# Kernel tuning notes

Hardware: AMD Instinct MI355X
Metric: run time of the kernel (lower is better)

The kernel has to match this reference:

```python
import jax, jax.numpy as jnp
import numpy as np

HIDDEN = 2048
HEADS = 16
HEAD_DIM = HIDDEN // HEADS
THETA = 10000.0


def _rope(x, seq_len):
    # x: [B, S, H, Dh]; standard rotate-half RoPE (cos1==cos2, sin1==sin2 in source)
    d = x.shape[-1]
    inv_freq = 1.0 / (THETA ** (jnp.arange(0, d, 2, dtype=jnp.float32) / d))  # [Dh/2]
    freqs = jnp.arange(seq_len, dtype=jnp.float32)[:, None] * inv_freq[None, :]  # [S, Dh/2]
    cos = jnp.cos(freqs)[None, :, None, :]  # [1,S,1,Dh/2]
    sin = jnp.sin(freqs)[None, :, None, :]
    x1, x2 = x[..., : d // 2], x[..., d // 2 :]
    return jnp.concatenate([x1 * cos - x2 * sin, x1 * sin + x2 * cos], axis=-1)


def setup_inputs() -> dict:
    key = jax.random.key(0)
    ks = jax.random.split(key, 5)
    B, S = 2, 2048
    scale = 1.0 / np.sqrt(HIDDEN)
    return {
        "x": jax.random.normal(ks[0], (B, S, HIDDEN), dtype=jnp.float32),
        "Wq": jax.random.normal(ks[1], (HIDDEN, HIDDEN), dtype=jnp.float32) * scale,
        "Wk": jax.random.normal(ks[2], (HIDDEN, HIDDEN), dtype=jnp.float32) * scale,
        "Wv": jax.random.normal(ks[3], (HIDDEN, HIDDEN), dtype=jnp.float32) * scale,
        "Wo": jax.random.normal(ks[4], (HIDDEN, HIDDEN), dtype=jnp.float32) * scale,
    }


def reference(x, Wq, Wk, Wv, Wo):
    B, S, _ = x.shape
    # nn.Linear(bias=False): y = x @ W.T
    q = (x @ Wq.T).reshape(B, S, HEADS, HEAD_DIM)
    k = (x @ Wk.T).reshape(B, S, HEADS, HEAD_DIM)
    v = (x @ Wv.T).reshape(B, S, HEADS, HEAD_DIM)
    q = _rope(q, S)
    k = _rope(k, S)
    # [B,H,S,S] scores
    scores = jnp.einsum("bqhd,bkhd->bhqk", q, k) / jnp.sqrt(jnp.float32(HEAD_DIM))
    attn = jax.nn.softmax(scores, axis=-1)
    out = jnp.einsum("bhqk,bkhd->bqhd", attn, v).reshape(B, S, HIDDEN)
    return out @ Wo.T
```

## Files before the change

kernel.cpp:

```cpp
#include <hip/hip_runtime.h>
#include <hip/hip_bf16.h>


typedef __attribute__((ext_vector_type(8))) short short8;
typedef __attribute__((ext_vector_type(4))) float f32x4;
typedef __attribute__((ext_vector_type(4))) unsigned short us4;
typedef __attribute__((ext_vector_type(4))) unsigned int u32x4;

__device__ __forceinline__ void gll16(const void* g, void* l) {
  __builtin_amdgcn_global_load_lds((const __attribute__((address_space(1))) void*)g,
                                   (__attribute__((address_space(3))) void*)l, 16, 0, 0);
}

__device__ __forceinline__ unsigned short f2bf(float f) {
  __hip_bfloat16 h = __float2bfloat16(f);
  return *reinterpret_cast<unsigned short*>(&h);
}

__device__ __forceinline__ float bf2f(short s) {
  union { unsigned int u; float f; } c;
  c.u = ((unsigned int)(unsigned short)s) << 16;
  return c.f;
}

__device__ __forceinline__ unsigned int cvtpk(float lo, float hi) {
  unsigned int r;
  asm("v_cvt_pk_bf16_f32 %0, %1, %2" : "=v"(r) : "v"(lo), "v"(hi));
  return r;
}

__device__ __forceinline__ void xcd_remap(int& Bx, int& By) {
  const int flat = blockIdx.y * gridDim.x + blockIdx.x;
  const int xcd = flat & 7, idx = flat >> 3;
  const int ppx = gridDim.y >> 3;
  By = xcd * ppx + (idx % ppx);
  Bx = idx / ppx;
}

__global__ __launch_bounds__(256) void cast5(const float* __restrict__ x,
                                             const float* __restrict__ wq,
                                             const float* __restrict__ wk,
                                             const float* __restrict__ wv,
                                             const float* __restrict__ wo,
                                             __hip_bfloat16* __restrict__ xb,
                                             __hip_bfloat16* __restrict__ dq,
                                             __hip_bfloat16* __restrict__ dk,
                                             __hip_bfloat16* __restrict__ dv,
                                             __hip_bfloat16* __restrict__ dwo,
                                             int nx4, int nw4) {
  int i = blockIdx.x * 256 + threadIdx.x;
  const float* in;
  __hip_bfloat16* out;
  int j = i;
  if (i < nx4) { in = x; out = xb; }
  else if ((j = i - nx4) < nw4) { in = wq; out = dq; }
  else if ((j -= nw4) < nw4) { in = wk; out = dk; }
  else if ((j -= nw4) < nw4) { in = wv; out = dv; }
  else if ((j -= nw4) < nw4) { in = wo; out = dwo; }
  else return;
  const float4 v = reinterpret_cast<const float4*>(in)[j];
  us4 o;
  o[0] = f2bf(v.x); o[1] = f2bf(v.y); o[2] = f2bf(v.z); o[3] = f2bf(v.w);
  *reinterpret_cast<us4*>(out + (size_t)j * 4) = o;
}

template <typename EPI>
__device__ __forceinline__ void gemm_core(const __hip_bfloat16* A, const __hip_bfloat16* Bt,
                                          int row0, int col0, int K, EPI epi) {
  __shared__ char As[2][16384];
  __shared__ char Bs[2][16384];
  const int tid = threadIdx.x;
  const int lane = tid & 63, wid = tid >> 6;
  const int l15 = lane & 15, l4 = lane >> 4;
  const int wm = (wid >> 1) * 64, wn = (wid & 1) * 64;

  f32x4 acc[4][4] = {};

  const int rs = lane >> 3;
  const int cs = lane & 7;
  const int cg = cs ^ rs;
  const char* Ab = (const char*)A;
  const char* Bb = (const char*)Bt;
  const size_t Kb = (size_t)K * 2;
  const int NT = K >> 6;

#define GSTAGE(T, S)                                                                      \
  {                                                                                       \
    const int k0_ = (T) << 6;                                                             \
    _Pragma("unroll") for (int c_ = 0; c_ < 4; ++c_) {                                    \
      const int cid_ = wid * 4 + c_;                                                      \
      const int r_ = cid_ * 8 + rs;                                                       \
      gll16(Ab + (size_t)(row0 + r_) * Kb + (size_t)k0_ * 2 + cg * 16, As[S] + cid_ * 1024); \
      gll16(Bb + (size_t)(col0 + r_) * Kb + (size_t)k0_ * 2 + cg * 16, Bs[S] + cid_ * 1024); \
    }                                                                                     \
  }

  GSTAGE(0, 0);
  GSTAGE(1, 1);
  asm volatile("s_waitcnt vmcnt(8)" ::: "memory");
  __builtin_amdgcn_s_barrier();

  for (int t = 0; t < NT; ++t) {
    const int s = t & 1;
    short8 a[2][4], b[2][4];
#pragma unroll
    for (int kc = 0; kc < 2; ++kc)
#pragma unroll
      for (int i = 0; i < 4; ++i) {
        const int ra = wm + i * 16 + l15;
        a[kc][i] = *(const short8*)(As[s] + ra * 128 + (((kc * 4 + l4) ^ (ra & 7)) * 16));
        const int rb = wn + i * 16 + l15;
        b[kc][i] = *(const short8*)(Bs[s] + rb * 128 + (((kc * 4 + l4) ^ (rb & 7)) * 16));
      }
    asm volatile("s_waitcnt lgkmcnt(0)" ::: "memory");
    __builtin_amdgcn_sched_barrier(0);
    __builtin_amdgcn_s_barrier();
    if (t + 2 < NT) {
      GSTAGE(t + 2, s);
      asm volatile("s_waitcnt vmcnt(8)" ::: "memory");
    } else if (t + 2 == NT) {
      asm volatile("s_waitcnt vmcnt(0)" ::: "memory");
    }
    __builtin_amdgcn_s_barrier();
#pragma unroll
    for (int kc = 0; kc < 2; ++kc) {
      __builtin_amdgcn_s_setprio(1);
#pragma unroll
      for (int i = 0; i < 4; ++i)
#pragma unroll
        for (int j = 0; j < 4; ++j)
          acc[i][j] = __builtin_amdgcn_mfma_f32_16x16x32_bf16(a[kc][i], b[kc][j], acc[i][j], 0, 0, 0);
      __builtin_amdgcn_s_setprio(0);
    }
  }
  epi(acc, wm, wn, l15, l4);
#undef GSTAGE
}

template <int MODE>
__global__ __launch_bounds__(256) void gemm_bt(const __hip_bfloat16* __restrict__ A,
                                               const __hip_bfloat16* __restrict__ Bt,
                                               void* __restrict__ Cout,
                                               int M, int N, int K) {
  int Bx, By;
  xcd_remap(Bx, By);
  const int row0 = Bx * 128, col0 = By * 128;
  gemm_core(A, Bt, row0, col0, K, [=](f32x4 (&acc)[4][4], int wm, int wn, int l15, int l4) {
    if (MODE == 2) {
      __hip_bfloat16* vt = (__hip_bfloat16*)Cout;
#pragma unroll
      for (int i = 0; i < 4; ++i) {
        const int gm = row0 + wm + i * 16 + l4 * 4;
        const int bb = gm >> 11, kvb = gm & 2047;
        const int phys = (kvb & ~31) + (((kvb >> 2) & 3) << 3) + (((kvb >> 4) & 1) << 2);
#pragma unroll
        for (int j = 0; j < 4; ++j) {
          const int gn = col0 + wn + j * 16 + l15;
          const int h = gn >> 7, d = gn & 127;
          us4 o;
          o[0] = f2bf(acc[i][j][0]); o[1] = f2bf(acc[i][j][1]);
          o[2] = f2bf(acc[i][j][2]); o[3] = f2bf(acc[i][j][3]);
          *reinterpret_cast<us4*>(vt + ((size_t)((bb * 16 + h) * 128 + d) * 2048 + phys)) = o;
        }
      }
    } else {
#pragma unroll
      for (int i = 0; i < 4; ++i)
#pragma unroll
        for (int j = 0; j < 4; ++j) {
          const int gn = col0 + wn + j * 16 + l15;
#pragma unroll
          for (int r = 0; r < 4; ++r) {
            const int gm = row0 + wm + i * 16 + l4 * 4 + r;
            if (MODE == 0)
              ((__hip_bfloat16*)Cout)[(size_t)gm * N + gn] = __float2bfloat16(acc[i][j][r]);
            else
              ((float*)Cout)[(size_t)gm * N + gn] = acc[i][j][r];
          }
        }
    }
  });
}

__global__ __launch_bounds__(256) void gemm_qkv(const __hip_bfloat16* __restrict__ A,
                                                const __hip_bfloat16* __restrict__ Wq,
                                                const __hip_bfloat16* __restrict__ Wk,
                                                const __hip_bfloat16* __restrict__ Wv,
                                                __hip_bfloat16* __restrict__ qb,
                                                __hip_bfloat16* __restrict__ kb,
                                                __hip_bfloat16* __restrict__ vtb) {
  int Bx, By;
  xcd_remap(Bx, By);
  const int row0 = Bx * 128;
  const int sel = By >> 4;
  const int col0 = (By & 15) * 128;
  const __hip_bfloat16* Bt = (sel == 0) ? Wq : (sel == 1) ? Wk : Wv;
  __hip_bfloat16* outq = (sel == 0) ? qb : kb;

  gemm_core(A, Bt, row0, col0, 2048, [=](f32x4 (&acc)[4][4], int wm, int wn, int l15, int l4) {
    if (sel == 2) {
#pragma unroll
      for (int i = 0; i < 4; ++i) {
        const int gm = row0 + wm + i * 16 + l4 * 4;
        const int bb = gm >> 11, kvb = gm & 2047;
        const int phys = (kvb & ~31) + (((kvb >> 2) & 3) << 3) + (((kvb >> 4) & 1) << 2);
#pragma unroll
        for (int j = 0; j < 4; ++j) {
          const int gn = col0 + wn + j * 16 + l15;
          const int h = gn >> 7, d = gn & 127;
          us4 o;
          o[0] = f2bf(acc[i][j][0]); o[1] = f2bf(acc[i][j][1]);
          o[2] = f2bf(acc[i][j][2]); o[3] = f2bf(acc[i][j][3]);
          *reinterpret_cast<us4*>(vtb + ((size_t)((bb * 16 + h) * 128 + d) * 2048 + phys)) = o;
        }
      }
    } else {
#pragma unroll
      for (int i = 0; i < 4; ++i)
#pragma unroll
        for (int j = 0; j < 4; ++j) {
          const int gn = col0 + wn + j * 16 + l15;
#pragma unroll
          for (int r = 0; r < 4; ++r) {
            const int gm = row0 + wm + i * 16 + l4 * 4 + r;
            outq[(size_t)gm * 2048 + gn] = __float2bfloat16(acc[i][j][r]);
          }
        }
    }
  });
}

__global__ __launch_bounds__(256) void rope_k(__hip_bfloat16* __restrict__ q,
                                              __hip_bfloat16* __restrict__ k) {
  const int tid = blockIdx.x * 256 + threadIdx.x;
  const int i8 = tid & 7;
  const int h = (tid >> 3) & 15;
  const int row = (tid >> 7) & 4095;
  const int isk = tid >> 19;
  __hip_bfloat16* p = isk ? k : q;
  const float qs = isk ? 1.0f : 0.1275224187f;
  const int pos = row & 2047;
  const size_t base = (size_t)row * 2048 + h * 128 + i8 * 8;
  const short8 v1 = *reinterpret_cast<const short8*>(p + base);
  const short8 v2 = *reinterpret_cast<const short8*>(p + base + 64);
  short8 o1, o2;
#pragma unroll
  for (int j = 0; j < 8; ++j) {
    const int i = i8 * 8 + j;
    const float invf = exp2f((float)i * -0.20762050593046f);
    const float fr = (float)pos * invf;
    float sv, cv;
    sincosf(fr, &sv, &cv);
    const float x1 = bf2f(v1[j]), x2 = bf2f(v2[j]);
    o1[j] = (short)f2bf((x1 * cv - x2 * sv) * qs);
    o2[j] = (short)f2bf((x1 * sv + x2 * cv) * qs);
  }
  *reinterpret_cast<short8*>(p + base) = o1;
  *reinterpret_cast<short8*>(p + base + 64) = o2;
}

__global__ __launch_bounds__(256) void flash_k(const __hip_bfloat16* __restrict__ q,
                                               const __hip_bfloat16* __restrict__ k,
                                               const __hip_bfloat16* __restrict__ vt,
                                               __hip_bfloat16* __restrict__ ao) {
  __shared__ char Ks[2][16384];
  __shared__ char VTs[2][16384];
  const int tid = threadIdx.x, lane = tid & 63, wid = tid >> 6;
  const int bx = blockIdx.x;
  const int qt = bx >> 5, bh = bx & 31, b = bh >> 4, h = bh & 15;
  const int l15 = lane & 15, l4 = lane >> 4;

  short8 qf[2][4];
  const char* qB = (const char*)q;
#pragma unroll
  for (int mi = 0; mi < 2; ++mi)
#pragma unroll
    for (int kc = 0; kc < 4; ++kc) {
      const size_t off =
          ((size_t)(b * 2048 + qt * 128 + wid * 32 + mi * 16 + l15) * 2048 + h * 128 + kc * 32 + l4 * 8) * 2;
      qf[mi][kc] = *(const short8*)(qB + off);
    }

  f32x4 oacc[2][8] = {};
  f32x4 lracc[2] = {};

  const short8 ones = {(short)0x3F80, (short)0x3F80, (short)0x3F80, (short)0x3F80,
                       (short)0x3F80, (short)0x3F80, (short)0x3F80, (short)0x3F80};

  const char* kbase = (const char*)k + ((size_t)(b * 2048) * 2048 + h * 128) * 2;
  const char* vtbase = (const char*)vt + ((size_t)bh * 128 * 2048) * 2;

  const int krow = lane >> 4, kcol = lane & 15;
  const int vrow = lane >> 3, vcol = lane & 7;

#define GSTAGE(T, S)                                                                          \
  {                                                                                           \
    const int kv0_ = (T)*64;                                                                  \
    _Pragma("unroll") for (int c_ = 0; c_ < 4; ++c_) {                                        \
      const int cid_ = wid * 4 + c_;                                                          \
      const int rk_ = cid_ * 4 + krow;                                                        \
      gll16(kbase + (size_t)(kv0_ + rk_) * 4096 + ((kcol ^ (rk_ & 7)) * 16),                  \
            Ks[S] + cid_ * 1024);                                                             \
      const int rv_ = cid_ * 8 + vrow;                                                        \
      gll16(vtbase + (size_t)rv_ * 4096 + (size_t)kv0_ * 2 + ((vcol ^ (rv_ & 7)) * 16),       \
            VTs[S] + cid_ * 1024);                                                            \
    }                                                                                         \
  }

  GSTAGE(0, 0);
  GSTAGE(1, 1);
  asm volatile("s_waitcnt vmcnt(8)" ::: "memory");
  __builtin_amdgcn_s_barrier();

  for (int t = 0; t < 32; ++t) {
    const int s = t & 1;

    f32x4 sacc[2][4] = {};
#pragma unroll
    for (int kc = 0; kc < 4; ++kc) {
      short8 kf[4];
#pragma unroll
      for (int ni = 0; ni < 4; ++ni) {
        const int r = ni * 16 + l15;
        kf[ni] = *(const short8*)(Ks[s] + r * 256 + (((kc * 4 + l4) ^ (r & 7)) * 16));
      }
#pragma unroll
      for (int mi = 0; mi < 2; ++mi)
#pragma unroll
        for (int ni = 0; ni < 4; ++ni)
          sacc[mi][ni] = __builtin_amdgcn_mfma_f32_16x16x32_bf16(kf[ni], qf[mi][kc], sacc[mi][ni], 0, 0, 0);
    }

    unsigned int W[2][4][2];
#pragma unroll
    for (int mi = 0; mi < 2; ++mi)
#pragma unroll
      for (int ni = 0; ni < 4; ++ni) {
        W[mi][ni][0] = cvtpk(exp2f(sacc[mi][ni][0]), exp2f(sacc[mi][ni][1]));
        W[mi][ni][1] = cvtpk(exp2f(sacc[mi][ni][2]), exp2f(sacc[mi][ni][3]));
      }

#pragma unroll
    for (int kc = 0; kc < 2; ++kc) {
      union { u32x4 u; short8 s; } pfu[2];
#pragma unroll
      for (int mi = 0; mi < 2; ++mi) {
        pfu[mi].u[0] = W[mi][kc * 2][0];
        pfu[mi].u[1] = W[mi][kc * 2][1];
        pfu[mi].u[2] = W[mi][kc * 2 + 1][0];
        pfu[mi].u[3] = W[mi][kc * 2 + 1][1];
      }
#pragma unroll
      for (int nd = 0; nd < 8; ++nd) {
        const int r = nd * 16 + l15;
        const short8 vf = *(const short8*)(
            VTs[s] + r * 128 + (((kc * 4 + l4) ^ (r & 7)) * 16));
#pragma unroll
        for (int mi = 0; mi < 2; ++mi)
          oacc[mi][nd] = __builtin_amdgcn_mfma_f32_16x16x32_bf16(vf, pfu[mi].s, oacc[mi][nd], 0, 0, 0);
      }
#pragma unroll
      for (int mi = 0; mi < 2; ++mi)
        lracc[mi] = __builtin_amdgcn_mfma_f32_16x16x32_bf16(ones, pfu[mi].s, lracc[mi], 0, 0, 0);
    }

    asm volatile("s_waitcnt lgkmcnt(0)" ::: "memory");
    __builtin_amdgcn_sched_barrier(0);
    __builtin_amdgcn_s_barrier();
    if (t + 2 < 32) {
      GSTAGE(t + 2, s);
      asm volatile("s_waitcnt vmcnt(8)" ::: "memory");
    } else if (t + 2 == 32) {
      asm volatile("s_waitcnt vmcnt(0)" ::: "memory");
    }
    __builtin_amdgcn_s_barrier();
  }

#pragma unroll
  for (int mi = 0; mi < 2; ++mi) {
    const float inv = 1.f / lracc[mi][0];
    const int qrow = qt * 128 + wid * 32 + mi * 16 + l15;
    const size_t rowoff = ((size_t)(b * 2048 + qrow)) * 2048 + h * 128;
#pragma unroll
    for (int nd = 0; nd < 8; ++nd) {
      us4 o;
      o[0] = f2bf(oacc[mi][nd][0] * inv);
      o[1] = f2bf(oacc[mi][nd][1] * inv);
      o[2] = f2bf(oacc[mi][nd][2] * inv);
      o[3] = f2bf(oacc[mi][nd][3] * inv);
      *reinterpret_cast<us4*>(ao + rowoff + nd * 16 + l4 * 4) = o;
    }
  }
#undef GSTAGE
}

extern "C" void kernel_launch(void* const* d_in, const int* in_sizes, int n_in,
                              void* d_out, int out_size, void* d_ws, size_t ws_size,
                              hipStream_t stream) {
  const float* x  = (const float*)d_in[0];
  const float* Wq = (const float*)d_in[1];
  const float* Wk = (const float*)d_in[2];
  const float* Wv = (const float*)d_in[3];
  const float* Wo = (const float*)d_in[4];
  float* out = (float*)d_out;

  const size_t MK = (size_t)4096 * 2048;
  const size_t WN = (size_t)2048 * 2048;
  if (ws_size < (4 * MK + WN) * 2) return;

  __hip_bfloat16* ws  = (__hip_bfloat16*)d_ws;
  __hip_bfloat16* xb  = ws;
  __hip_bfloat16* qb  = ws + MK;
  __hip_bfloat16* kb  = ws + 2 * MK;
  __hip_bfloat16* vtb = ws + 3 * MK;
  __hip_bfloat16* wsl = ws + 4 * MK;
  __hip_bfloat16* aob = xb;
  __hip_bfloat16* dq = (__hip_bfloat16*)d_out;
  __hip_bfloat16* dk = dq + WN;
  __hip_bfloat16* dv = dk + WN;

  const int nx4 = (int)(MK / 4), nw4 = (int)(WN / 4);
  cast5<<<dim3((nx4 + 4 * nw4) / 256), 256, 0, stream>>>(x, Wq, Wk, Wv, Wo,
                                                         xb, dq, dk, dv, wsl, nx4, nw4);
  gemm_qkv<<<dim3(32, 48), 256, 0, stream>>>(xb, dq, dk, dv, qb, kb, vtb);
  rope_k<<<4096, 256, 0, stream>>>(qb, kb);
  flash_k<<<512, 256, 0, stream>>>(qb, kb, vtb, aob);
  gemm_bt<1><<<dim3(32, 16), 256, 0, stream>>>(aob, wsl, out, 4096, 2048, 2048);
}
```

Baseline: 254.6 us.

## Fuse RoPE and query scaling into QKV GEMM epilogue via LDS exchange

Applies RoPE and the query softmax scale inside the Q/K GEMM epilogue and removes the separate rope kernel. Warp pairs holding the two halves of each head swap accumulators through a 16 KB shared buffer, so each thread can rotate its values with the partner half. This removes one kernel launch and a full read-modify-write pass over Q and K in global memory. In exchange it adds shared memory and block-wide barriers in the epilogue, plus sincos work done per element inside the GEMM.

Measured after the change: 308.3 us. 21.1% more time.

```diff
diff --git a/kernel.cpp b/kernel.cpp
--- a/kernel.cpp
+++ b/kernel.cpp
@@ -189,6 +189,7 @@
                                                 __hip_bfloat16* __restrict__ qb,
                                                 __hip_bfloat16* __restrict__ kb,
                                                 __hip_bfloat16* __restrict__ vtb) {
+  __shared__ char xch[16384];
   int Bx, By;
   xcd_remap(Bx, By);
   const int row0 = Bx * 128;
@@ -196,6 +197,7 @@
   const int col0 = (By & 15) * 128;
   const __hip_bfloat16* Bt = (sel == 0) ? Wq : (sel == 1) ? Wk : Wv;
   __hip_bfloat16* outq = (sel == 0) ? qb : kb;
+  char* xchp = xch;
 
   gemm_core(A, Bt, row0, col0, 2048, [=](f32x4 (&acc)[4][4], int wm, int wn, int l15, int l4) {
     if (sel == 2) {
@@ -215,48 +217,42 @@
         }
       }
     } else {
-#pragma unroll
-      for (int i = 0; i < 4; ++i)
+      const int wid = threadIdx.x >> 6, lane = threadIdx.x & 63;
+      const float qs = (sel == 0) ? 0.1275224187f : 1.0f;
+      const int lo_half = (wn == 0);
+#pragma unroll
+      for (int i = 0; i < 4; ++i) {
+#pragma unroll
+        for (int j = 0; j < 4; ++j)
+          *(f32x4*)(xchp + wid * 4096 + j * 1024 + lane * 16) = acc[i][j];
+        __syncthreads();
+        f32x4 pacc[4];
+#pragma unroll
+        for (int j = 0; j < 4; ++j)
+          pacc[j] = *(const f32x4*)(xchp + (wid ^ 1) * 4096 + j * 1024 + lane * 16);
 #pragma unroll
         for (int j = 0; j < 4; ++j) {
+          const int ii = j * 16 + l15;
+          const float invf = exp2f((float)ii * -0.20762050593046f);
           const int gn = col0 + wn + j * 16 + l15;
 #pragma unroll
           for (int r = 0; r < 4; ++r) {
             const int gm = row0 + wm + i * 16 + l4 * 4 + r;
-            outq[(size_t)gm * 2048 + gn] = __float2bfloat16(acc[i][j][r]);
+            const int pos = gm & 2047;
+            float sv, cv;
+            sincosf((float)pos * invf, &sv, &cv);
+            const float mine = acc[i][j][r], other = pacc[j][r];
+            const float ov = lo_half ? (mine * cv - other * sv) * qs
+                                     : (other * sv + mine * cv) * qs;
+            union { unsigned short u; __hip_bfloat16 h; } cvt;
+            cvt.u = f2bf(ov);
+            outq[(size_t)gm * 2048 + gn] = cvt.h;
           }
         }
+        __syncthreads();
+      }
     }
   });
-}
-
-__global__ __launch_bounds__(256) void rope_k(__hip_bfloat16* __restrict__ q,
-                                              __hip_bfloat16* __restrict__ k) {
-  const int tid = blockIdx.x * 256 + threadIdx.x;
-  const int i8 = tid & 7;
-  const int h = (tid >> 3) & 15;
-  const int row = (tid >> 7) & 4095;
-  const int isk = tid >> 19;
-  __hip_bfloat16* p = isk ? k : q;
-  const float qs = isk ? 1.0f : 0.1275224187f;
-  const int pos = row & 2047;
-  const size_t base = (size_t)row * 2048 + h * 128 + i8 * 8;
-  const short8 v1 = *reinterpret_cast<const short8*>(p + base);
-  const short8 v2 = *reinterpret_cast<const short8*>(p + base + 64);
-  short8 o1, o2;
-#pragma unroll
-  for (int j = 0; j < 8; ++j) {
-    const int i = i8 * 8 + j;
-    const float invf = exp2f((float)i * -0.20762050593046f);
-    const float fr = (float)pos * invf;
-    float sv, cv;
-    sincosf(fr, &sv, &cv);
-    const float x1 = bf2f(v1[j]), x2 = bf2f(v2[j]);
-    o1[j] = (short)f2bf((x1 * cv - x2 * sv) * qs);
-    o2[j] = (short)f2bf((x1 * sv + x2 * cv) * qs);
-  }
-  *reinterpret_cast<short8*>(p + base) = o1;
-  *reinterpret_cast<short8*>(p + base + 64) = o2;
 }
 
 __global__ __launch_bounds__(256) void flash_k(const __hip_bfloat16* __restrict__ q,
@@ -423,7 +419,6 @@
   cast5<<<dim3((nx4 + 4 * nw4) / 256), 256, 0, stream>>>(x, Wq, Wk, Wv, Wo,
                                                          xb, dq, dk, dv, wsl, nx4, nw4);
   gemm_qkv<<<dim3(32, 48), 256, 0, stream>>>(xb, dq, dk, dv, qb, kb, vtb);
-  rope_k<<<4096, 256, 0, stream>>>(qb, kb);
   flash_k<<<512, 256, 0, stream>>>(qb, kb, vtb, aob);
   gemm_bt<1><<<dim3(32, 16), 256, 0, stream>>>(aob, wsl, out, 4096, 2048, 2048);
 }
```
